# Kernel optimization log

Measured on AMD Instinct MI355X. Metric: run time of the kernel, lower is better.

The kernel has to match this reference:

```python
import jax, jax.numpy as jnp
import numpy as np
import math

B, S = 8, 2048
N_HIDDEN_RNN = 512
D_MODEL = 1024
NUM_HEADS = 16
N_OUTPUT = 1024
SCALE = math.sqrt(D_MODEL // NUM_HEADS)  # head_dim used only for scaling


def setup_inputs() -> dict:
    key = jax.random.key(0)
    ks = jax.random.split(key, 11)
    def lin(k, fan_in, fan_out):
        bound = 1.0 / math.sqrt(fan_in)
        kw, kb = jax.random.split(k)
        W = jax.random.uniform(kw, (fan_out, fan_in), jnp.float32, -bound, bound)
        b = jax.random.uniform(kb, (fan_out,), jnp.float32, -bound, bound)
        return W, b
    Wq, bq = lin(ks[0], N_HIDDEN_RNN, D_MODEL)
    Wk, bk = lin(ks[1], D_MODEL, D_MODEL)
    Wv, bv = lin(ks[2], D_MODEL, D_MODEL)
    Wo, bo = lin(ks[3], D_MODEL, N_OUTPUT)
    return {
        "query": jax.random.normal(ks[4], (B, S, N_HIDDEN_RNN), jnp.float32),
        "key": jax.random.normal(ks[5], (B, S, D_MODEL), jnp.float32),
        "value": jax.random.normal(ks[6], (B, S, D_MODEL), jnp.float32),
        "Wq": Wq, "bq": bq, "Wk": Wk, "bk": bk,
        "Wv": Wv, "bv": bv, "Wo": Wo, "bo": bo,
    }


def reference(query, key, value, Wq, bq, Wk, bk, Wv, bv, Wo, bo):
    # Projections
    q = query @ Wq.T + bq      # [B, S, d_model]
    k = key @ Wk.T + bk        # [B, S, d_model]
    v = value @ Wv.T + bv      # [B, S, d_model]
    # Original code transposes to [B, d_model, S] (feature-axis attention).
    # scores[b, i, j] = sum_s q[b, s, i] * k[b, s, j] / scale -> [B, d, d]
    scores = jnp.einsum('bsi,bsj->bij', q, k) / SCALE
    probs = jax.nn.softmax(scores, axis=-1)   # softmax over feature axis j
    # out[b, s, i] = sum_j probs[b, i, j] * v[b, s, j]
    attn_out = jnp.einsum('bij,bsj->bsi', probs, v)  # [B, S, d_model]
    return attn_out @ Wo.T + bo  # [B, S, n_output]
```

## Files before the change

kernel.cpp:

```cpp
#include <hip/hip_runtime.h>
#include <hip/hip_bf16.h>
#include <stdint.h>

typedef __bf16 b16x8 __attribute__((ext_vector_type(8)));
typedef float  f32x4 __attribute__((ext_vector_type(4)));

__device__ __forceinline__ unsigned short f2bf(float f) {
    uint32_t u = __float_as_uint(f);
    u += 0x7fffu + ((u >> 16) & 1u);
    return (unsigned short)(u >> 16);
}
__device__ __forceinline__ float bf2f(unsigned short s) {
    return __uint_as_float(((uint32_t)s) << 16);
}

__device__ __forceinline__ void gld16(const unsigned short* g, unsigned short* l) {
    __builtin_amdgcn_global_load_lds(
        (const __attribute__((address_space(1))) void*)g,
        (__attribute__((address_space(3))) void*)l, 16, 0, 0);
}

__global__ void k_detect(const unsigned short* __restrict__ q, int n, int* __restrict__ flag) {
    float m = 0.f;
    for (int i = threadIdx.x; i < n; i += 256) {
        float f = fabsf(bf2f(q[i]));
        if (!(f < 1e30f)) f = 1e30f;
        m = fmaxf(m, f);
    }
#pragma unroll
    for (int o = 32; o > 0; o >>= 1) m = fmaxf(m, __shfl_xor(m, o));
    __shared__ float red[4];
    if ((threadIdx.x & 63) == 0) red[threadIdx.x >> 6] = m;
    __syncthreads();
    if (threadIdx.x == 0) {
        m = fmaxf(fmaxf(red[0], red[1]), fmaxf(red[2], red[3]));
        flag[0] = (m > 1e6f) ? 1 : 0;
    }
}

__global__ __launch_bounds__(256) void k_cvt(const void* __restrict__ src,
                                             unsigned short* __restrict__ dst,
                                             long n8, const int* __restrict__ flag) {
    long i = blockIdx.x * 256L + threadIdx.x;
    long stride = (long)gridDim.x * 256L;
    if (flag[0]) {
        const float4* s = (const float4*)src;
        for (long j = i; j < n8; j += stride) {
            float4 a = s[2 * j], b = s[2 * j + 1];
            uint4 o;
            o.x = f2bf(a.x) | ((uint32_t)f2bf(a.y) << 16);
            o.y = f2bf(a.z) | ((uint32_t)f2bf(a.w) << 16);
            o.z = f2bf(b.x) | ((uint32_t)f2bf(b.y) << 16);
            o.w = f2bf(b.z) | ((uint32_t)f2bf(b.w) << 16);
            ((uint4*)dst)[j] = o;
        }
    } else {
        const uint4* s = (const uint4*)src;
        for (long j = i; j < n8; j += stride) ((uint4*)dst)[j] = s[j];
    }
}

__global__ __launch_bounds__(256) void k_cvt_bias(const void* b0, const void* b1,
                                                  const void* b2, const void* b3,
                                                  float* __restrict__ dst,
                                                  const int* __restrict__ flag) {
    int i = blockIdx.x * 256 + threadIdx.x;
    int which = i >> 10, idx = i & 1023;
    const void* src = (which == 0) ? b0 : (which == 1) ? b1 : (which == 2) ? b2 : b3;
    dst[i] = flag[0] ? ((const float*)src)[idx] : bf2f(((const unsigned short*)src)[idx]);
}

template <int MODE>
__global__ __launch_bounds__(512, 2) void k_gemm3(
    const unsigned short* __restrict__ A, const unsigned short* __restrict__ B,
    const float* __restrict__ bias, void* __restrict__ Cv,
    int N, int K, int ldA, int ldB, int lb,
    long sAb, long sBb, long sCb, float scale,
    const int* __restrict__ flagp)
{
    extern __shared__ unsigned short lds_raw[];
    const int tid  = threadIdx.x;
    const int lane = tid & 63;
    const int wave = tid >> 6;
    const int nwg = gridDim.x * gridDim.y;
    const int bid = blockIdx.y * gridDim.x + blockIdx.x;
    const int nq  = nwg >> 3;
    const int vb  = (bid & 7) * nq + (bid >> 3);
    const int bn  = (vb & (gridDim.x - 1)) * 256;
    const int bm  = (vb / gridDim.x) * 256;
    const int batch = bm >> lb;
    const int am0 = bm & ((1 << lb) - 1);
    const int Mb = 1 << lb;
    const unsigned short* Ab = A + (long)batch * sAb;
    const unsigned short* Bb = B + (long)batch * sBb;
    const long zC = (long)batch * sCb;
    const int g  = wave >> 2;
    const int wn = (wave & 3) * 64;

    f32x4 acc[8][4];
    const f32x4 zero = {0.f, 0.f, 0.f, 0.f};
#pragma unroll
    for (int i = 0; i < 8; ++i)
#pragma unroll
        for (int j = 0; j < 4; ++j) acc[i][j] = zero;

    auto stageQ = [&](int kt, int cb, int q) {
        unsigned short* Lbase = lds_raw + (size_t)cb * 32768 + ((q < 2) ? 16384 : 0);
#pragma unroll
        for (int j = 0; j < 2; ++j) {
            const int c = (q & 1) * 1024 + j * 512 + tid;
            const int row = c >> 3;
            const int klo = (c & 7) ^ (row & 7);
            if (q < 2)
                gld16(Bb + (long)(bn + row) * ldB + kt * 64 + klo * 8, Lbase + (size_t)c * 8);
            else
                gld16(Ab + (long)(am0 + row) * ldA + kt * 64 + klo * 8, Lbase + (size_t)c * 8);
        }
    };

    const int NT = K >> 6;
#pragma unroll
    for (int q = 0; q < 4; ++q) stageQ(0, 0, q);

    int cur = 0;
    for (int t = 0; t < NT; ++t) {
        const int has_next = (t + 1 < NT);
        const unsigned short* LA = lds_raw + (size_t)cur * 32768;
        const unsigned short* LB = LA + 16384;
        b16x8 bfr[4][2];
#pragma unroll
        for (int p = 0; p < 4; ++p) {
            if (p == 0) {
                asm volatile("s_waitcnt vmcnt(2)" ::: "memory");
            } else if (p == 2) {
                if (has_next) asm volatile("s_waitcnt vmcnt(4)" ::: "memory");
                else          asm volatile("s_waitcnt vmcnt(0)" ::: "memory");
            }
            __builtin_amdgcn_sched_barrier(0);
            __builtin_amdgcn_s_barrier();
            asm volatile("" ::: "memory");
            if (p == 0) {
#pragma unroll
                for (int j = 0; j < 4; ++j)
#pragma unroll
                    for (int s = 0; s < 2; ++s) {
                        const int r = wn + j * 16 + (lane & 15);
                        const int kl = s * 4 + (lane >> 4);
                        bfr[j][s] = *(const b16x8*)(LB + ((size_t)r * 8 + (kl ^ (r & 7))) * 8);
                    }
            }
            b16x8 afr[2][2];
#pragma unroll
            for (int r = 0; r < 2; ++r)
#pragma unroll
                for (int s = 0; s < 2; ++s) {
                    const int row = (p >> 1) * 128 + (p & 1) * 64 + g * 32 + r * 16 + (lane & 15);
                    const int kl = s * 4 + (lane >> 4);
                    afr[r][s] = *(const b16x8*)(LA + ((size_t)row * 8 + (kl ^ (row & 7))) * 8);
                }
            if (has_next) stageQ(t + 1, cur ^ 1, p);
            asm volatile("" ::: "memory");
            __builtin_amdgcn_s_barrier();
            __builtin_amdgcn_sched_barrier(0);
            __builtin_amdgcn_s_setprio(1);
#pragma unroll
            for (int r = 0; r < 2; ++r)
#pragma unroll
                for (int j = 0; j < 4; ++j)
#pragma unroll
                    for (int s = 0; s < 2; ++s)
                        acc[p * 2 + r][j] = __builtin_amdgcn_mfma_f32_16x16x32_bf16(
                            afr[r][s], bfr[j][s], acc[p * 2 + r][j], 0, 0, 0);
            __builtin_amdgcn_s_setprio(0);
        }
        cur ^= 1;
    }

    const int fl = flagp ? flagp[0] : 1;
#pragma unroll
    for (int i = 0; i < 8; ++i) {
        const int p = i >> 1, r = i & 1;
        const int rloc = am0 + (p >> 1) * 128 + (p & 1) * 64 + g * 32 + r * 16 + (lane >> 4) * 4;
#pragma unroll
        for (int j = 0; j < 4; ++j) {
            const int n = bn + wn + j * 16 + (lane & 15);
            const float bv = (MODE != 2 && bias != nullptr) ? bias[n] : 0.f;
            if (MODE == 0) {
                unsigned short* C = (unsigned short*)Cv;
#pragma unroll
                for (int rr = 0; rr < 4; ++rr)
                    C[zC + (long)(rloc + rr) * N + n] = f2bf(acc[i][j][rr] * scale + bv);
            } else if (MODE == 1) {
                unsigned short* C = (unsigned short*)Cv;
                uint32_t p0 = f2bf(acc[i][j][0] * scale + bv) |
                              ((uint32_t)f2bf(acc[i][j][1] * scale + bv) << 16);
                uint32_t p1 = f2bf(acc[i][j][2] * scale + bv) |
                              ((uint32_t)f2bf(acc[i][j][3] * scale + bv) << 16);
                uint2 val; val.x = p0; val.y = p1;
                *(uint2*)(C + zC + (long)n * Mb + rloc) = val;
            } else if (MODE == 2) {
                float* C = (float*)Cv;
#pragma unroll
                for (int rr = 0; rr < 4; ++rr)
                    C[zC + (long)(rloc + rr) * N + n] = acc[i][j][rr] * scale;
            } else {
                if (fl) {
                    float* C = (float*)Cv;
#pragma unroll
                    for (int rr = 0; rr < 4; ++rr)
                        C[zC + (long)(rloc + rr) * N + n] = acc[i][j][rr] * scale + bv;
                } else {
                    unsigned short* C = (unsigned short*)Cv;
#pragma unroll
                    for (int rr = 0; rr < 4; ++rr)
                        C[zC + (long)(rloc + rr) * N + n] = f2bf(acc[i][j][rr] * scale + bv);
                }
            }
        }
    }
}

__global__ __launch_bounds__(256) void k_softmax(float* __restrict__ S) {
    const long row = blockIdx.x;
    float* s = S + row * 1024;
    unsigned short* p = (unsigned short*)s;
    const int tid = threadIdx.x;
    float4 v = ((const float4*)s)[tid];
    float m = fmaxf(fmaxf(v.x, v.y), fmaxf(v.z, v.w));
#pragma unroll
    for (int o = 32; o > 0; o >>= 1) m = fmaxf(m, __shfl_xor(m, o));
    __shared__ float sm[4], ss[4];
    if ((tid & 63) == 0) sm[tid >> 6] = m;
    __syncthreads();
    m = fmaxf(fmaxf(sm[0], sm[1]), fmaxf(sm[2], sm[3]));
    float e0 = __expf(v.x - m), e1 = __expf(v.y - m);
    float e2 = __expf(v.z - m), e3 = __expf(v.w - m);
    float sum = e0 + e1 + e2 + e3;
#pragma unroll
    for (int o = 32; o > 0; o >>= 1) sum += __shfl_xor(sum, o);
    if ((tid & 63) == 0) ss[tid >> 6] = sum;
    __syncthreads();
    float inv = 1.f / (ss[0] + ss[1] + ss[2] + ss[3]);
    uint32_t w0 = f2bf(e0 * inv) | ((uint32_t)f2bf(e1 * inv) << 16);
    uint32_t w1 = f2bf(e2 * inv) | ((uint32_t)f2bf(e3 * inv) << 16);
    uint2 val; val.x = w0; val.y = w1;
    *(uint2*)(p + tid * 4) = val;
}

extern "C" void kernel_launch(void* const* d_in, const int* in_sizes, int n_in,
                              void* d_out, int out_size, void* d_ws, size_t ws_size,
                              hipStream_t stream) {
    (void)in_sizes; (void)n_in; (void)out_size; (void)ws_size;
    const void* q_in = d_in[0];
    const void* k_in = d_in[1];
    const void* v_in = d_in[2];
    const void* Wq   = d_in[3];
    const void* bq   = d_in[4];
    const void* Wk   = d_in[5];
    const void* bk   = d_in[6];
    const void* Wv   = d_in[7];
    const void* bv   = d_in[8];
    const void* Wo   = d_in[9];
    const void* bo   = d_in[10];

    const size_t MB = 1u << 20;
    const size_t LDSB = 131072;
    hipFuncSetAttribute((const void*)k_gemm3<0>, hipFuncAttributeMaxDynamicSharedMemorySize, (int)LDSB);
    hipFuncSetAttribute((const void*)k_gemm3<1>, hipFuncAttributeMaxDynamicSharedMemorySize, (int)LDSB);
    hipFuncSetAttribute((const void*)k_gemm3<2>, hipFuncAttributeMaxDynamicSharedMemorySize, (int)LDSB);
    hipFuncSetAttribute((const void*)k_gemm3<3>, hipFuncAttributeMaxDynamicSharedMemorySize, (int)LDSB);

    char* ws = (char*)d_ws;
    int*            flag = (int*)ws;
    unsigned short* R1   = (unsigned short*)(ws + 1 * MB);
    unsigned short* R2   = (unsigned short*)(ws + 33 * MB);
    char*           R3   = ws + 65 * MB;
    unsigned short* kb = R1, *qb = R1, *vb = R1;
    unsigned short* Kt = R2, *attn = R2;
    float*          scores = (float*)R1;
    unsigned short* P      = R1;
    unsigned short* wqb = (unsigned short*)R3;
    unsigned short* wkb = (unsigned short*)(R3 + 1 * MB);
    unsigned short* wvb = (unsigned short*)(R3 + 3 * MB);
    unsigned short* wob = (unsigned short*)(R3 + 5 * MB);
    float*          bias4 = (float*)(R3 + 7 * MB);
    unsigned short* Vp = (unsigned short*)d_out;
    unsigned short* Qt = (unsigned short*)((char*)d_out + 32 * MB);

    dim3 blk(256);
    k_detect<<<1, blk, 0, stream>>>((const unsigned short*)q_in, 4096, flag);
    k_cvt_bias<<<16, blk, 0, stream>>>(bq, bk, bv, bo, bias4, flag);
    k_cvt<<<256, blk, 0, stream>>>(Wq, wqb, 1024L * 512 / 8, flag);
    k_cvt<<<512, blk, 0, stream>>>(Wk, wkb, 1024L * 1024 / 8, flag);
    k_cvt<<<512, blk, 0, stream>>>(Wv, wvb, 1024L * 1024 / 8, flag);
    k_cvt<<<512, blk, 0, stream>>>(Wo, wob, 1024L * 1024 / 8, flag);

    dim3 blk5(512);
    k_cvt<<<2048, blk, 0, stream>>>(k_in, kb, 8L * 2048 * 1024 / 8, flag);
    k_gemm3<1><<<dim3(4, 64), blk5, LDSB, stream>>>(
        kb, wkb, bias4 + 1024, Kt, 1024, 1024, 1024, 1024, 11,
        2048L * 1024, 0, 1024L * 2048, 1.f, nullptr);
    k_cvt<<<2048, blk, 0, stream>>>(q_in, qb, 8L * 2048 * 512 / 8, flag);
    k_gemm3<1><<<dim3(4, 64), blk5, LDSB, stream>>>(
        qb, wqb, bias4, Qt, 1024, 512, 512, 512, 11,
        2048L * 512, 0, 1024L * 2048, 1.f, nullptr);
    k_cvt<<<2048, blk, 0, stream>>>(v_in, vb, 8L * 2048 * 1024 / 8, flag);
    k_gemm3<0><<<dim3(4, 64), blk5, LDSB, stream>>>(
        vb, wvb, bias4 + 2 * 1024, Vp, 1024, 1024, 1024, 1024, 24,
        0, 0, 0, 1.f, nullptr);
    k_gemm3<2><<<dim3(4, 32), blk5, LDSB, stream>>>(
        Qt, Kt, nullptr, scores, 1024, 2048, 2048, 2048, 10,
        1024L * 2048, 1024L * 2048, 1024L * 1024, 0.125f, nullptr);
    k_softmax<<<dim3(8192), blk, 0, stream>>>(scores);
    k_gemm3<0><<<dim3(4, 64), blk5, LDSB, stream>>>(
        Vp, P, nullptr, attn, 1024, 1024, 1024, 2048, 11,
        2048L * 1024, 1024L * 2048, 2048L * 1024, 1.f, nullptr);
    k_gemm3<3><<<dim3(4, 64), blk5, LDSB, stream>>>(
        attn, wob, bias4 + 3 * 1024, d_out, 1024, 1024, 1024, 1024, 24,
        0, 0, 0, 1.f, flag);
}
```

Before: 319.0 us.

## Split GEMM into specialized kernels with simpler pipelines and smaller-tile variant

Replaces the single quarter-staged GEMM with three variants. k_gemmA is a plain double-buffered 256x256x64 kernel with an XOR-swizzled LDS layout. k_gemmB is a 128x256x32 tile kernel with 48KB LDS and 4 blocks per CU, used for the K and Q projections that write transposed output. k_gemmC keeps the original pipelined body but is specialized to bf16 output for the P*V product. The aim is better occupancy and less scheduling overhead, at the risk of losing the finer-grained overlap of the original staged pipeline.

```diff
diff --git a/kernel.cpp b/kernel.cpp
--- a/kernel.cpp
+++ b/kernel.cpp
@@ -71,7 +71,7 @@
 }
 
 template <int MODE>
-__global__ __launch_bounds__(512, 2) void k_gemm3(
+__global__ __launch_bounds__(512, 2) void k_gemmA(
     const unsigned short* __restrict__ A, const unsigned short* __restrict__ B,
     const float* __restrict__ bias, void* __restrict__ Cv,
     int N, int K, int ldA, int ldB, int lb,
@@ -84,13 +84,258 @@
     const int wave = tid >> 6;
     const int nwg = gridDim.x * gridDim.y;
     const int bid = blockIdx.y * gridDim.x + blockIdx.x;
-    const int nq  = nwg >> 3;
-    const int vb  = (bid & 7) * nq + (bid >> 3);
+    const int vb  = (bid & 7) * (nwg >> 3) + (bid >> 3);
     const int bn  = (vb & (gridDim.x - 1)) * 256;
     const int bm  = (vb / gridDim.x) * 256;
     const int batch = bm >> lb;
     const int am0 = bm & ((1 << lb) - 1);
     const int Mb = 1 << lb;
+    const unsigned short* Ab = A + (long)batch * sAb;
+    const unsigned short* Bb = B + (long)batch * sBb;
+    const long zC = (long)batch * sCb;
+    const int wm = (wave >> 2) * 128;
+    const int wn = (wave & 3) * 64;
+
+    f32x4 acc[8][4];
+    const f32x4 zero = {0.f, 0.f, 0.f, 0.f};
+#pragma unroll
+    for (int i = 0; i < 8; ++i)
+#pragma unroll
+        for (int j = 0; j < 4; ++j) acc[i][j] = zero;
+
+    auto stage = [&](int kt, int cb) {
+        unsigned short* LA = lds_raw + (size_t)cb * 32768;
+        unsigned short* LB = LA + 16384;
+#pragma unroll
+        for (int j = 0; j < 4; ++j) {
+            const int d = j * 512 + tid;
+            const int row = d >> 3;
+            const int klo = (d & 7) ^ (row & 7);
+            gld16(Ab + (long)(am0 + row) * ldA + kt * 64 + klo * 8, LA + (size_t)d * 8);
+            gld16(Bb + (long)(bn + row) * ldB + kt * 64 + klo * 8, LB + (size_t)d * 8);
+        }
+    };
+    auto ctile = [&](int cb) {
+        const unsigned short* LA = lds_raw + (size_t)cb * 32768;
+        const unsigned short* LB = LA + 16384;
+        b16x8 bfr[4][2];
+#pragma unroll
+        for (int p = 0; p < 4; ++p) {
+            if (p == 0) {
+#pragma unroll
+                for (int j = 0; j < 4; ++j)
+#pragma unroll
+                    for (int s = 0; s < 2; ++s) {
+                        const int r = wn + j * 16 + (lane & 15);
+                        const int kl = s * 4 + (lane >> 4);
+                        bfr[j][s] = *(const b16x8*)(LB + ((size_t)r * 8 + (kl ^ (r & 7))) * 8);
+                    }
+            }
+            b16x8 a[2][2];
+#pragma unroll
+            for (int q = 0; q < 2; ++q)
+#pragma unroll
+                for (int s = 0; s < 2; ++s) {
+                    const int r = wm + (2 * p + q) * 16 + (lane & 15);
+                    const int kl = s * 4 + (lane >> 4);
+                    a[q][s] = *(const b16x8*)(LA + ((size_t)r * 8 + (kl ^ (r & 7))) * 8);
+                }
+            __builtin_amdgcn_s_setprio(1);
+#pragma unroll
+            for (int q = 0; q < 2; ++q)
+#pragma unroll
+                for (int j = 0; j < 4; ++j)
+#pragma unroll
+                    for (int s = 0; s < 2; ++s)
+                        acc[2 * p + q][j] = __builtin_amdgcn_mfma_f32_16x16x32_bf16(
+                            a[q][s], bfr[j][s], acc[2 * p + q][j], 0, 0, 0);
+            __builtin_amdgcn_s_setprio(0);
+        }
+    };
+
+    const int NT = K >> 6;
+    stage(0, 0);
+    __syncthreads();
+    int cur = 0;
+    for (int kt = 0; kt < NT - 1; ++kt) {
+        stage(kt + 1, cur ^ 1);
+        ctile(cur);
+        __syncthreads();
+        cur ^= 1;
+    }
+    ctile(cur);
+
+    const int fl = flagp ? flagp[0] : 1;
+#pragma unroll
+    for (int i = 0; i < 8; ++i)
+#pragma unroll
+        for (int j = 0; j < 4; ++j) {
+            const int rloc = am0 + wm + i * 16 + (lane >> 4) * 4;
+            const int n    = bn + wn + j * 16 + (lane & 15);
+            const float bv = (MODE != 2 && bias != nullptr) ? bias[n] : 0.f;
+            if (MODE == 0) {
+                unsigned short* C = (unsigned short*)Cv;
+#pragma unroll
+                for (int r = 0; r < 4; ++r)
+                    C[zC + (long)(rloc + r) * N + n] = f2bf(acc[i][j][r] * scale + bv);
+            } else if (MODE == 1) {
+                unsigned short* C = (unsigned short*)Cv;
+                uint32_t p0 = f2bf(acc[i][j][0] * scale + bv) |
+                              ((uint32_t)f2bf(acc[i][j][1] * scale + bv) << 16);
+                uint32_t p1 = f2bf(acc[i][j][2] * scale + bv) |
+                              ((uint32_t)f2bf(acc[i][j][3] * scale + bv) << 16);
+                uint2 val; val.x = p0; val.y = p1;
+                *(uint2*)(C + zC + (long)n * Mb + rloc) = val;
+            } else if (MODE == 2) {
+                float* C = (float*)Cv;
+#pragma unroll
+                for (int r = 0; r < 4; ++r)
+                    C[zC + (long)(rloc + r) * N + n] = acc[i][j][r] * scale;
+            } else {
+                if (fl) {
+                    float* C = (float*)Cv;
+#pragma unroll
+                    for (int r = 0; r < 4; ++r)
+                        C[zC + (long)(rloc + r) * N + n] = acc[i][j][r] * scale + bv;
+                } else {
+                    unsigned short* C = (unsigned short*)Cv;
+#pragma unroll
+                    for (int r = 0; r < 4; ++r)
+                        C[zC + (long)(rloc + r) * N + n] = f2bf(acc[i][j][r] * scale + bv);
+                }
+            }
+        }
+}
+
+template <int MODE>
+__global__ __launch_bounds__(512, 4) void k_gemmB(
+    const unsigned short* __restrict__ A, const unsigned short* __restrict__ B,
+    const float* __restrict__ bias, void* __restrict__ Cv,
+    int N, int K, int ldA, int ldB, int lb,
+    long sAb, long sBb, long sCb, float scale)
+{
+    extern __shared__ unsigned short lds_raw[];
+    const int tid  = threadIdx.x;
+    const int lane = tid & 63;
+    const int wave = tid >> 6;
+    const int nwg = gridDim.x * gridDim.y;
+    const int bid = blockIdx.y * gridDim.x + blockIdx.x;
+    const int vb  = (bid & 7) * (nwg >> 3) + (bid >> 3);
+    const int bn  = (vb & (gridDim.x - 1)) * 256;
+    const int bm  = (vb / gridDim.x) * 128;
+    const int batch = bm >> lb;
+    const int am0 = bm & ((1 << lb) - 1);
+    const int Mb = 1 << lb;
+    const unsigned short* Ab = A + (long)batch * sAb;
+    const unsigned short* Bb = B + (long)batch * sBb;
+    const long zC = (long)batch * sCb;
+    const int wm = (wave >> 2) * 64;
+    const int wn = (wave & 3) * 64;
+
+    f32x4 acc[4][4];
+    const f32x4 zero = {0.f, 0.f, 0.f, 0.f};
+#pragma unroll
+    for (int i = 0; i < 4; ++i)
+#pragma unroll
+        for (int j = 0; j < 4; ++j) acc[i][j] = zero;
+
+    auto stage = [&](int kt, int cb) {
+        unsigned short* Lb = lds_raw + (size_t)cb * 12288;
+        {
+            const int c = tid, row = c >> 2;
+            const int klo = (c & 3) ^ ((row >> 1) & 3);
+            gld16(Ab + (long)(am0 + row) * ldA + kt * 32 + klo * 8, Lb + (size_t)c * 8);
+        }
+#pragma unroll
+        for (int j = 0; j < 2; ++j) {
+            const int c = j * 512 + tid, row = c >> 2;
+            const int klo = (c & 3) ^ ((row >> 1) & 3);
+            gld16(Bb + (long)(bn + row) * ldB + kt * 32 + klo * 8, Lb + 4096 + (size_t)c * 8);
+        }
+    };
+    auto ctile = [&](int cb) {
+        const unsigned short* LA = lds_raw + (size_t)cb * 12288;
+        const unsigned short* LB = LA + 4096;
+        const int kl = lane >> 4;
+        b16x8 af[4], bf[4];
+#pragma unroll
+        for (int j = 0; j < 4; ++j) {
+            const int r = wn + j * 16 + (lane & 15);
+            bf[j] = *(const b16x8*)(LB + ((size_t)r * 4 + (kl ^ ((r >> 1) & 3))) * 8);
+        }
+#pragma unroll
+        for (int i = 0; i < 4; ++i) {
+            const int r = wm + i * 16 + (lane & 15);
+            af[i] = *(const b16x8*)(LA + ((size_t)r * 4 + (kl ^ ((r >> 1) & 3))) * 8);
+        }
+        __builtin_amdgcn_s_setprio(1);
+#pragma unroll
+        for (int i = 0; i < 4; ++i)
+#pragma unroll
+            for (int j = 0; j < 4; ++j)
+                acc[i][j] = __builtin_amdgcn_mfma_f32_16x16x32_bf16(af[i], bf[j], acc[i][j], 0, 0, 0);
+        __builtin_amdgcn_s_setprio(0);
+    };
+
+    const int NT = K >> 5;
+    stage(0, 0);
+    __syncthreads();
+    int cur = 0;
+    for (int kt = 0; kt < NT - 1; ++kt) {
+        stage(kt + 1, cur ^ 1);
+        ctile(cur);
+        __syncthreads();
+        cur ^= 1;
+    }
+    ctile(cur);
+
+#pragma unroll
+    for (int i = 0; i < 4; ++i)
+#pragma unroll
+        for (int j = 0; j < 4; ++j) {
+            const int rloc = am0 + wm + i * 16 + (lane >> 4) * 4;
+            const int n    = bn + wn + j * 16 + (lane & 15);
+            const float bv = (MODE != 2 && bias != nullptr) ? bias[n] : 0.f;
+            if (MODE == 0) {
+                unsigned short* C = (unsigned short*)Cv;
+#pragma unroll
+                for (int r = 0; r < 4; ++r)
+                    C[zC + (long)(rloc + r) * N + n] = f2bf(acc[i][j][r] * scale + bv);
+            } else if (MODE == 1) {
+                unsigned short* C = (unsigned short*)Cv;
+                uint32_t p0 = f2bf(acc[i][j][0] * scale + bv) |
+                              ((uint32_t)f2bf(acc[i][j][1] * scale + bv) << 16);
+                uint32_t p1 = f2bf(acc[i][j][2] * scale + bv) |
+                              ((uint32_t)f2bf(acc[i][j][3] * scale + bv) << 16);
+                uint2 val; val.x = p0; val.y = p1;
+                *(uint2*)(C + zC + (long)n * Mb + rloc) = val;
+            } else {
+                float* C = (float*)Cv;
+#pragma unroll
+                for (int r = 0; r < 4; ++r)
+                    C[zC + (long)(rloc + r) * N + n] = acc[i][j][r] * scale;
+            }
+        }
+}
+
+template <int MODE>
+__global__ __launch_bounds__(512, 2) void k_gemmC(
+    const unsigned short* __restrict__ A, const unsigned short* __restrict__ B,
+    const float* __restrict__ bias, void* __restrict__ Cv,
+    int N, int K, int ldA, int ldB, int lb,
+    long sAb, long sBb, long sCb, float scale)
+{
+    extern __shared__ unsigned short lds_raw[];
+    const int tid  = threadIdx.x;
+    const int lane = tid & 63;
+    const int wave = tid >> 6;
+    const int nwg = gridDim.x * gridDim.y;
+    const int bid = blockIdx.y * gridDim.x + blockIdx.x;
+    const int vb  = (bid & 7) * (nwg >> 3) + (bid >> 3);
+    const int bn  = (vb & (gridDim.x - 1)) * 256;
+    const int bm  = (vb / gridDim.x) * 256;
+    const int batch = bm >> lb;
+    const int am0 = bm & ((1 << lb) - 1);
     const unsigned short* Ab = A + (long)batch * sAb;
     const unsigned short* Bb = B + (long)batch * sBb;
     const long zC = (long)batch * sCb;
@@ -176,7 +421,6 @@
         cur ^= 1;
     }
 
-    const int fl = flagp ? flagp[0] : 1;
 #pragma unroll
     for (int i = 0; i < 8; ++i) {
         const int p = i >> 1, r = i & 1;
@@ -184,38 +428,11 @@
 #pragma unroll
         for (int j = 0; j < 4; ++j) {
             const int n = bn + wn + j * 16 + (lane & 15);
-            const float bv = (MODE != 2 && bias != nullptr) ? bias[n] : 0.f;
-            if (MODE == 0) {
-                unsigned short* C = (unsigned short*)Cv;
-#pragma unroll
-                for (int rr = 0; rr < 4; ++rr)
-                    C[zC + (long)(rloc + rr) * N + n] = f2bf(acc[i][j][rr] * scale + bv);
-            } else if (MODE == 1) {
-                unsigned short* C = (unsigned short*)Cv;
-                uint32_t p0 = f2bf(acc[i][j][0] * scale + bv) |
-                              ((uint32_t)f2bf(acc[i][j][1] * scale + bv) << 16);
-                uint32_t p1 = f2bf(acc[i][j][2] * scale + bv) |
-                              ((uint32_t)f2bf(acc[i][j][3] * scale + bv) << 16);
-                uint2 val; val.x = p0; val.y = p1;
-                *(uint2*)(C + zC + (long)n * Mb + rloc) = val;
-            } else if (MODE == 2) {
-                float* C = (float*)Cv;
-#pragma unroll
-                for (int rr = 0; rr < 4; ++rr)
-                    C[zC + (long)(rloc + rr) * N + n] = acc[i][j][rr] * scale;
-            } else {
-                if (fl) {
-                    float* C = (float*)Cv;
-#pragma unroll
-                    for (int rr = 0; rr < 4; ++rr)
-                        C[zC + (long)(rloc + rr) * N + n] = acc[i][j][rr] * scale + bv;
-                } else {
-                    unsigned short* C = (unsigned short*)Cv;
-#pragma unroll
-                    for (int rr = 0; rr < 4; ++rr)
-                        C[zC + (long)(rloc + rr) * N + n] = f2bf(acc[i][j][rr] * scale + bv);
-                }
-            }
+            const float bv = (bias != nullptr) ? bias[n] : 0.f;
+            unsigned short* C = (unsigned short*)Cv;
+#pragma unroll
+            for (int rr = 0; rr < 4; ++rr)
+                C[zC + (long)(rloc + rr) * N + n] = f2bf(acc[i][j][rr] * scale + bv);
         }
     }
 }
@@ -264,11 +481,12 @@
     const void* bo   = d_in[10];
 
     const size_t MB = 1u << 20;
-    const size_t LDSB = 131072;
-    hipFuncSetAttribute((const void*)k_gemm3<0>, hipFuncAttributeMaxDynamicSharedMemorySize, (int)LDSB);
-    hipFuncSetAttribute((const void*)k_gemm3<1>, hipFuncAttributeMaxDynamicSharedMemorySize, (int)LDSB);
-    hipFuncSetAttribute((const void*)k_gemm3<2>, hipFuncAttributeMaxDynamicSharedMemorySize, (int)LDSB);
-    hipFuncSetAttribute((const void*)k_gemm3<3>, hipFuncAttributeMaxDynamicSharedMemorySize, (int)LDSB);
+    const size_t LDS_A = 131072, LDS_B = 49152;
+    hipFuncSetAttribute((const void*)k_gemmA<0>, hipFuncAttributeMaxDynamicSharedMemorySize, (int)LDS_A);
+    hipFuncSetAttribute((const void*)k_gemmA<2>, hipFuncAttributeMaxDynamicSharedMemorySize, (int)LDS_A);
+    hipFuncSetAttribute((const void*)k_gemmA<3>, hipFuncAttributeMaxDynamicSharedMemorySize, (int)LDS_A);
+    hipFuncSetAttribute((const void*)k_gemmB<1>, hipFuncAttributeMaxDynamicSharedMemorySize, (int)LDS_B);
+    hipFuncSetAttribute((const void*)k_gemmC<0>, hipFuncAttributeMaxDynamicSharedMemorySize, (int)LDS_A);
 
     char* ws = (char*)d_ws;
     int*            flag = (int*)ws;
@@ -287,7 +505,7 @@
     unsigned short* Vp = (unsigned short*)d_out;
     unsigned short* Qt = (unsigned short*)((char*)d_out + 32 * MB);
 
-    dim3 blk(256);
+    dim3 blk(256), blk5(512);
     k_detect<<<1, blk, 0, stream>>>((const unsigned short*)q_in, 4096, flag);
     k_cvt_bias<<<16, blk, 0, stream>>>(bq, bk, bv, bo, bias4, flag);
     k_cvt<<<256, blk, 0, stream>>>(Wq, wqb, 1024L * 512 / 8, flag);
@@ -295,27 +513,26 @@
     k_cvt<<<512, blk, 0, stream>>>(Wv, wvb, 1024L * 1024 / 8, flag);
     k_cvt<<<512, blk, 0, stream>>>(Wo, wob, 1024L * 1024 / 8, flag);
 
-    dim3 blk5(512);
     k_cvt<<<2048, blk, 0, stream>>>(k_in, kb, 8L * 2048 * 1024 / 8, flag);
-    k_gemm3<1><<<dim3(4, 64), blk5, LDSB, stream>>>(
+    k_gemmB<1><<<dim3(4, 128), blk5, LDS_B, stream>>>(
         kb, wkb, bias4 + 1024, Kt, 1024, 1024, 1024, 1024, 11,
-        2048L * 1024, 0, 1024L * 2048, 1.f, nullptr);
+        2048L * 1024, 0, 1024L * 2048, 1.f);
     k_cvt<<<2048, blk, 0, stream>>>(q_in, qb, 8L * 2048 * 512 / 8, flag);
-    k_gemm3<1><<<dim3(4, 64), blk5, LDSB, stream>>>(
+    k_gemmB<1><<<dim3(4, 128), blk5, LDS_B, stream>>>(
         qb, wqb, bias4, Qt, 1024, 512, 512, 512, 11,
-        2048L * 512, 0, 1024L * 2048, 1.f, nullptr);
+        2048L * 512, 0, 1024L * 2048, 1.f);
     k_cvt<<<2048, blk, 0, stream>>>(v_in, vb, 8L * 2048 * 1024 / 8, flag);
-    k_gemm3<0><<<dim3(4, 64), blk5, LDSB, stream>>>(
+    k_gemmA<0><<<dim3(4, 64), blk5, LDS_A, stream>>>(
         vb, wvb, bias4 + 2 * 1024, Vp, 1024, 1024, 1024, 1024, 24,
         0, 0, 0, 1.f, nullptr);
-    k_gemm3<2><<<dim3(4, 32), blk5, LDSB, stream>>>(
+    k_gemmA<2><<<dim3(4, 32), blk5, LDS_A, stream>>>(
         Qt, Kt, nullptr, scores, 1024, 2048, 2048, 2048, 10,
         1024L * 2048, 1024L * 2048, 1024L * 1024, 0.125f, nullptr);
     k_softmax<<<dim3(8192), blk, 0, stream>>>(scores);
-    k_gemm3<0><<<dim3(4, 64), blk5, LDSB, stream>>>(
+    k_gemmC<0><<<dim3(4, 64), blk5, LDS_A, stream>>>(
         Vp, P, nullptr, attn, 1024, 1024, 1024, 2048, 11,
-        2048L * 1024, 1024L * 2048, 2048L * 1024, 1.f, nullptr);
-    k_gemm3<3><<<dim3(4, 64), blk5, LDSB, stream>>>(
+        2048L * 1024, 1024L * 2048, 2048L * 1024, 1.f);
+    k_gemmA<3><<<dim3(4, 64), blk5, LDS_A, stream>>>(
         attn, wob, bias4 + 3 * 1024, d_out, 1024, 1024, 1024, 1024, 24,
         0, 0, 0, 1.f, flag);
 }
```

Measured after the change: 331.4 us. 3.9% more time.
